# Kernel optimization log

Measured on AMD Instinct MI355X. Metric: run time of the kernel, lower is better.

The kernel has to match this reference:

```python
import jax, jax.numpy as jnp
import numpy as np

DIM = 192
HEADS = 6
WS = 7          # window size
SHIFT = 3       # shift size
HID = 768       # mlp hidden
EPS = 1e-5


def _rel_pos_index(ws):
    coords = np.stack(np.meshgrid(np.arange(ws), np.arange(ws), indexing='ij'))  # (2, ws, ws)
    cf = coords.reshape(2, -1)                       # (2, ws*ws)
    rel = cf[:, :, None] - cf[:, None, :]            # (2, N, N)
    rel = rel.transpose(1, 2, 0).astype(np.int64)
    rel[:, :, 0] += ws - 1
    rel[:, :, 1] += ws - 1
    rel[:, :, 0] *= 2 * ws - 1
    return jnp.asarray(rel.sum(-1))                  # (N, N)

REL_IDX = _rel_pos_index(WS)


def _layernorm(x, w, b):
    mu = jnp.mean(x, axis=-1, keepdims=True)
    var = jnp.mean(jnp.square(x - mu), axis=-1, keepdims=True)
    return (x - mu) * jax.lax.rsqrt(var + EPS) * w + b


def setup_inputs() -> dict:
    key = jax.random.key(0)
    ks = jax.random.split(key, 8)
    B, H, W = 32, 56, 56
    s = 0.02
    return {
        'x': jax.random.normal(ks[0], (B, H * W, DIM), jnp.float32),
        'norm1_w': jnp.ones((DIM,), jnp.float32),
        'norm1_b': jnp.zeros((DIM,), jnp.float32),
        'qkv_w': jax.random.normal(ks[1], (3 * DIM, DIM), jnp.float32) * s,
        'qkv_b': jnp.zeros((3 * DIM,), jnp.float32),
        'rpb_table': jax.random.normal(ks[2], ((2 * WS - 1) ** 2, HEADS), jnp.float32) * s,
        'proj_w': jax.random.normal(ks[3], (DIM, DIM), jnp.float32) * s,
        'proj_b': jnp.zeros((DIM,), jnp.float32),
        'norm2_w': jnp.ones((DIM,), jnp.float32),
        'norm2_b': jnp.zeros((DIM,), jnp.float32),
        'fc1_w': jax.random.normal(ks[4], (HID, DIM), jnp.float32) * s,
        'fc1_b': jnp.zeros((HID,), jnp.float32),
        'fc2_w': jax.random.normal(ks[5], (DIM, HID), jnp.float32) * s,
        'fc2_b': jnp.zeros((DIM,), jnp.float32),
        'H': H,
        'W': W,
    }


def reference(x, norm1_w, norm1_b, qkv_w, qkv_b, rpb_table, proj_w, proj_b,
              norm2_w, norm2_b, fc1_w, fc1_b, fc2_w, fc2_b, H, W):
    B, L, C = x.shape
    d = C // HEADS
    scale = d ** -0.5
    N = WS * WS

    shortcut = x
    h = _layernorm(x, norm1_w, norm1_b).reshape(B, H, W, C)
    if SHIFT > 0:
        h = jnp.roll(h, shift=(-SHIFT, -SHIFT), axis=(1, 2))

    # window partition -> (B * nW, N, C)
    h = h.reshape(B, H // WS, WS, W // WS, WS, C).transpose(0, 1, 3, 2, 4, 5)
    hw = h.reshape(-1, N, C)

    # windowed attention (NOTE: the torch block never passes a shift mask)
    qkv = hw @ qkv_w.T + qkv_b                                    # (B_, N, 3C)
    qkv = qkv.reshape(-1, N, 3, HEADS, d).transpose(2, 0, 3, 1, 4)
    q, k, v = qkv[0] * scale, qkv[1], qkv[2]                      # (B_, h, N, d)
    attn = jnp.einsum('bhnd,bhmd->bhnm', q, k)
    bias = rpb_table[REL_IDX].transpose(2, 0, 1)                  # (h, N, N)
    attn = jax.nn.softmax(attn + bias[None], axis=-1)
    out = jnp.einsum('bhnm,bhmd->bhnd', attn, v)
    out = out.transpose(0, 2, 1, 3).reshape(-1, N, C)
    out = out @ proj_w.T + proj_b

    # window reverse -> (B, H, W, C)
    out = out.reshape(B, H // WS, W // WS, WS, WS, C).transpose(0, 1, 3, 2, 4, 5)
    out = out.reshape(B, H, W, C)
    if SHIFT > 0:
        out = jnp.roll(out, shift=(SHIFT, SHIFT), axis=(1, 2))

    x = shortcut + out.reshape(B, L, C)
    h2 = _layernorm(x, norm2_w, norm2_b)
    mlp = jax.nn.gelu(h2 @ fc1_w.T + fc1_b, approximate=False) @ fc2_w.T + fc2_b
    return x + mlp
```

## Files before the change

### kernel.cpp

```cpp
#include <hip/hip_runtime.h>
#include <hip/hip_bf16.h>
#include <cmath>

typedef float f32x4 __attribute__((ext_vector_type(4)));
typedef __bf16 bf16x8 __attribute__((ext_vector_type(8)));

#define WS_SZ 7
#define SHIFT 3
#define HGRID 56
#define C_DIM 192
#define NHEADS 6
#define HDIM 32
#define NTOK 100352
#define NWIN 2048

__device__ __forceinline__ int win_to_tok(int wrow) {
    int w = wrow / 49, i = wrow - w * 49;
    int b = w >> 6, rem = w & 63;
    int wy = rem >> 3, wx = rem & 7;
    int yi = i / 7, xi = i - yi * 7;
    int y = wy * 7 + yi + SHIFT; if (y >= HGRID) y -= HGRID;
    int x = wx * 7 + xi + SHIFT; if (x >= HGRID) x -= HGRID;
    return b * (HGRID * HGRID) + y * HGRID + x;
}

__global__ __launch_bounds__(256)
void cvt_kernel(const float* __restrict__ src, __bf16* __restrict__ dst, int n8)
{
    int idx = blockIdx.x * 256 + threadIdx.x;
    if (idx >= n8) return;
    float4 a = ((const float4*)src)[idx * 2];
    float4 b = ((const float4*)src)[idx * 2 + 1];
    bf16x8 o;
    o[0] = (__bf16)a.x; o[1] = (__bf16)a.y; o[2] = (__bf16)a.z; o[3] = (__bf16)a.w;
    o[4] = (__bf16)b.x; o[5] = (__bf16)b.y; o[6] = (__bf16)b.z; o[7] = (__bf16)b.w;
    ((bf16x8*)dst)[idx] = o;
}

__global__ __launch_bounds__(256)
void bias_expand_kernel(const float* __restrict__ rpb, float* __restrict__ bias_g)
{
    int idx = blockIdx.x * 256 + threadIdx.x;
    if (idx >= NHEADS * 2401) return;
    int h = idx / 2401, rem = idx - h * 2401;
    int i = rem / 49, j = rem - i * 49;
    int yi = i / 7, xi = i - yi * 7;
    int yj = j / 7, xj = j - yj * 7;
    int ri = (yi - yj + 6) * 13 + (xi - xj + 6);
    bias_g[idx] = rpb[ri * NHEADS + h];
}

template<int WINDOWED>
__global__ __launch_bounds__(256)
void ln_kernel(const float* __restrict__ x, const float* __restrict__ w,
               const float* __restrict__ b, __bf16* __restrict__ out)
{
    int r = blockIdx.x * 4 + (threadIdx.x >> 6);
    int lane = threadIdx.x & 63;
    int src = WINDOWED ? win_to_tok(r) : r;
    const float* xp = x + (size_t)src * C_DIM;
    float v0 = xp[lane], v1 = xp[lane + 64], v2 = xp[lane + 128];
    float s = v0 + v1 + v2;
    float sq = v0 * v0 + v1 * v1 + v2 * v2;
    #pragma unroll
    for (int off = 32; off; off >>= 1) {
        s  += __shfl_xor(s, off);
        sq += __shfl_xor(sq, off);
    }
    float mu = s * (1.f / C_DIM);
    float rs = rsqrtf(sq * (1.f / C_DIM) - mu * mu + 1e-5f);
    __bf16* op = out + (size_t)r * C_DIM;
    op[lane]       = (__bf16)((v0 - mu) * rs * w[lane]       + b[lane]);
    op[lane + 64]  = (__bf16)((v1 - mu) * rs * w[lane + 64]  + b[lane + 64]);
    op[lane + 128] = (__bf16)((v2 - mu) * rs * w[lane + 128] + b[lane + 128]);
}

template<int MODE, int WBF16>
__global__ __launch_bounds__(256)
void gemm_kernel(const __bf16* __restrict__ A, const void* __restrict__ W,
                 const float* __restrict__ bias, void* __restrict__ outp,
                 const float* __restrict__ resid, int N, int K)
{
    __shared__ __bf16 As[128 * 40];
    __shared__ __bf16 Bs[64 * 40];
    const int tid = threadIdx.x;
    const int wave = tid >> 6, lane = tid & 63;
    const int wm = wave >> 1, wn = wave & 1;
    const int l15 = lane & 15, q8 = (lane >> 4) << 3;
    const int m0 = blockIdx.x * 128, n0 = blockIdx.y * 64;

    f32x4 acc[4][2];
    f32x4 zero = {0.f, 0.f, 0.f, 0.f};
    #pragma unroll
    for (int i = 0; i < 4; i++)
        #pragma unroll
        for (int j = 0; j < 2; j++) acc[i][j] = zero;

    const int br = tid >> 2, bc = (tid & 3) << 3;
    for (int kt = 0; kt < K; kt += 32) {
        __syncthreads();
        #pragma unroll
        for (int it = 0; it < 2; it++) {
            int idx = it * 256 + tid;
            int r = idx >> 2, c = (idx & 3) << 3;
            *(uint4*)(&As[r * 40 + c]) =
                *(const uint4*)(A + (size_t)(m0 + r) * K + kt + c);
        }
        if (WBF16) {
            *(uint4*)(&Bs[br * 40 + bc]) =
                *(const uint4*)((const __bf16*)W + (size_t)(n0 + br) * K + kt + bc);
        } else {
            const float* src = (const float*)W + (size_t)(n0 + br) * K + kt + bc;
            float4 f0 = *(const float4*)src;
            float4 f1 = *(const float4*)(src + 4);
            bf16x8 vb;
            vb[0] = (__bf16)f0.x; vb[1] = (__bf16)f0.y;
            vb[2] = (__bf16)f0.z; vb[3] = (__bf16)f0.w;
            vb[4] = (__bf16)f1.x; vb[5] = (__bf16)f1.y;
            vb[6] = (__bf16)f1.z; vb[7] = (__bf16)f1.w;
            *(bf16x8*)(&Bs[br * 40 + bc]) = vb;
        }
        __syncthreads();
        bf16x8 af[4], bfr[2];
        #pragma unroll
        for (int fm = 0; fm < 4; fm++)
            af[fm] = *(const bf16x8*)(&As[(wm * 64 + fm * 16 + l15) * 40 + q8]);
        #pragma unroll
        for (int fn = 0; fn < 2; fn++)
            bfr[fn] = *(const bf16x8*)(&Bs[(wn * 32 + fn * 16 + l15) * 40 + q8]);
        #pragma unroll
        for (int fm = 0; fm < 4; fm++)
            #pragma unroll
            for (int fn = 0; fn < 2; fn++)
                acc[fm][fn] = __builtin_amdgcn_mfma_f32_16x16x32_bf16(
                    af[fm], bfr[fn], acc[fm][fn], 0, 0, 0);
    }

    const int l4 = lane >> 4;
    #pragma unroll
    for (int fm = 0; fm < 4; fm++) {
        #pragma unroll
        for (int fn = 0; fn < 2; fn++) {
            int c = n0 + wn * 32 + fn * 16 + l15;
            float bv = bias[c];
            #pragma unroll
            for (int r = 0; r < 4; r++) {
                int m = m0 + wm * 64 + fm * 16 + l4 * 4 + r;
                float v = acc[fm][fn][r] + bv;
                if (MODE == 0) {
                    ((__bf16*)outp)[(size_t)m * N + c] = (__bf16)v;
                } else if (MODE == 2) {
                    float g = 0.5f * v * (1.f + erff(v * 0.70710678118654752f));
                    ((__bf16*)outp)[(size_t)m * N + c] = (__bf16)g;
                } else if (MODE == 1) {
                    int t = win_to_tok(m);
                    ((float*)outp)[(size_t)t * C_DIM + c] =
                        resid[(size_t)t * C_DIM + c] + v;
                } else {
                    float* p = (float*)outp + (size_t)m * C_DIM + c;
                    *p = *p + v;
                }
            }
        }
    }
}

__global__ __launch_bounds__(256, 2)
void attn_mfma_kernel(const __bf16* __restrict__ qkv,
                      const float* __restrict__ bias_g,
                      __bf16* __restrict__ out)
{
    const int wave = threadIdx.x >> 6;
    const int lane = threadIdx.x & 63;
    const int pair = blockIdx.x * 4 + wave;
    const int w = pair / 6, head = pair - (pair / 6) * 6;

    __shared__ __bf16 vsT_s[4][32 * 72];
    __shared__ __bf16 Ps_s[4][64 * 72];
    __bf16* vsT = vsT_s[wave];
    __bf16* Ps  = Ps_s[wave];

    const int l15 = lane & 15, q4 = lane >> 4, q8 = q4 << 3;
    const size_t qbase = (size_t)w * 49 * 576 + head * 32;

    {
        int d = lane & 31, jh = lane >> 5;
        #pragma unroll
        for (int it = 0; it < 25; ++it) {
            int j = it * 2 + jh;
            if (j < 49)
                vsT[d * 72 + j] = qkv[qbase + (size_t)j * 576 + 384 + d];
        }
        for (int idx = lane; idx < 32 * 15; idx += 64) {
            int dd = idx / 15, jj = 49 + (idx - dd * 15);
            vsT[dd * 72 + jj] = (__bf16)0.f;
        }
    }

    bf16x8 qf[4], kf[4];
    #pragma unroll
    for (int t = 0; t < 4; ++t) {
        int row = t * 16 + l15;
        int rq = row < 49 ? row : 48;
        qf[t] = *(const bf16x8*)(qkv + qbase + (size_t)rq * 576 + q8);
        kf[t] = *(const bf16x8*)(qkv + qbase + (size_t)rq * 576 + 192 + q8);
    }

    f32x4 sc[4][4];
    f32x4 zero = {0.f, 0.f, 0.f, 0.f};
    #pragma unroll
    for (int tm = 0; tm < 4; ++tm)
        #pragma unroll
        for (int tn = 0; tn < 4; ++tn) sc[tm][tn] = zero;
    #pragma unroll
    for (int tm = 0; tm < 4; ++tm)
        #pragma unroll
        for (int tn = 0; tn < 4; ++tn)
            sc[tm][tn] = __builtin_amdgcn_mfma_f32_16x16x32_bf16(
                qf[tm], kf[tn], sc[tm][tn], 0, 0, 0);

    const float scale = 0.17677669529663687f;
    const int hbase = head * 2401;
    #pragma unroll
    for (int tm = 0; tm < 4; ++tm) {
        #pragma unroll
        for (int r = 0; r < 4; ++r) {
            int i = tm * 16 + q4 * 4 + r;
            int ioff = hbase + (i < 49 ? i : 48) * 49;
            float v[4];
            #pragma unroll
            for (int tn = 0; tn < 4; ++tn) {
                int j = tn * 16 + l15;
                float bz = (j < 49) ? bias_g[ioff + (j < 49 ? j : 0)] : 0.f;
                float t = sc[tm][tn][r] * scale + bz;
                v[tn] = (j < 49) ? t : -1e30f;
            }
            float mx = fmaxf(fmaxf(v[0], v[1]), fmaxf(v[2], v[3]));
            mx = fmaxf(mx, __shfl_xor(mx, 1));
            mx = fmaxf(mx, __shfl_xor(mx, 2));
            mx = fmaxf(mx, __shfl_xor(mx, 4));
            mx = fmaxf(mx, __shfl_xor(mx, 8));
            float sm = 0.f;
            #pragma unroll
            for (int tn = 0; tn < 4; ++tn) {
                float e = __expf(v[tn] - mx);
                sc[tm][tn][r] = e;
                sm += e;
            }
            sm += __shfl_xor(sm, 1);
            sm += __shfl_xor(sm, 2);
            sm += __shfl_xor(sm, 4);
            sm += __shfl_xor(sm, 8);
            float inv = 1.f / sm;
            if (i < 49) {
                #pragma unroll
                for (int tn = 0; tn < 4; ++tn) {
                    int j = tn * 16 + l15;
                    Ps[i * 72 + j] = (__bf16)((j < 49) ? sc[tm][tn][r] * inv : 0.f);
                }
            }
        }
    }

    __syncthreads();

    f32x4 oc[4][2];
    #pragma unroll
    for (int tm = 0; tm < 4; ++tm)
        #pragma unroll
        for (int tn = 0; tn < 2; ++tn) oc[tm][tn] = zero;
    #pragma unroll
    for (int ks = 0; ks < 2; ++ks) {
        bf16x8 bv[2];
        #pragma unroll
        for (int tn = 0; tn < 2; ++tn)
            bv[tn] = *(const bf16x8*)(vsT + (tn * 16 + l15) * 72 + ks * 32 + q8);
        #pragma unroll
        for (int tm = 0; tm < 4; ++tm) {
            bf16x8 ap = *(const bf16x8*)(Ps + (tm * 16 + l15) * 72 + ks * 32 + q8);
            #pragma unroll
            for (int tn = 0; tn < 2; ++tn)
                oc[tm][tn] = __builtin_amdgcn_mfma_f32_16x16x32_bf16(
                    ap, bv[tn], oc[tm][tn], 0, 0, 0);
        }
    }

    #pragma unroll
    for (int tm = 0; tm < 4; ++tm) {
        #pragma unroll
        for (int r = 0; r < 4; ++r) {
            int m = tm * 16 + q4 * 4 + r;
            if (m < 49) {
                __bf16* op = out + (size_t)(w * 49 + m) * C_DIM + head * 32;
                #pragma unroll
                for (int tn = 0; tn < 2; ++tn)
                    op[tn * 16 + l15] = (__bf16)(oc[tm][tn][r]);
            }
        }
    }
}

extern "C" void kernel_launch(void* const* d_in, const int* in_sizes, int n_in,
                              void* d_out, int out_size, void* d_ws, size_t ws_size,
                              hipStream_t stream) {
    const float* x     = (const float*)d_in[0];
    const float* n1w   = (const float*)d_in[1];
    const float* n1b   = (const float*)d_in[2];
    const float* qkvw  = (const float*)d_in[3];
    const float* qkvb  = (const float*)d_in[4];
    const float* rpb   = (const float*)d_in[5];
    const float* projw = (const float*)d_in[6];
    const float* projb = (const float*)d_in[7];
    const float* n2w   = (const float*)d_in[8];
    const float* n2b   = (const float*)d_in[9];
    const float* fc1w  = (const float*)d_in[10];
    const float* fc1b  = (const float*)d_in[11];
    const float* fc2w  = (const float*)d_in[12];
    const float* fc2b  = (const float*)d_in[13];
    float* out = (float*)d_out;
    char* ws = (char*)d_ws;

    __bf16* bufA = (__bf16*)ws;
    __bf16* bufQ = (__bf16*)(ws + 38535168);
    __bf16* bufH = (__bf16*)(ws + 38535168);
    __bf16* qkvw_b  = (__bf16*)(ws + 192151552);
    __bf16* projw_b = (__bf16*)(ws + 192151552 + 221184);
    float*  bias_g  = (float*) (ws + 192151552 + 221184 + 73728);

    cvt_kernel<<<(110592/8 + 255)/256, 256, 0, stream>>>(qkvw, qkvw_b, 110592/8);
    cvt_kernel<<<(36864/8  + 255)/256, 256, 0, stream>>>(projw, projw_b, 36864/8);
    bias_expand_kernel<<<(NHEADS*2401 + 255)/256, 256, 0, stream>>>(rpb, bias_g);

    ln_kernel<1><<<NTOK / 4, 256, 0, stream>>>(x, n1w, n1b, bufA);
    gemm_kernel<0, 1><<<dim3(NTOK / 128, 9), 256, 0, stream>>>(
        bufA, qkvw_b, qkvb, bufQ, nullptr, 576, 192);
    attn_mfma_kernel<<<NWIN * NHEADS / 4, 256, 0, stream>>>(bufQ, bias_g, bufA);
    gemm_kernel<1, 1><<<dim3(NTOK / 128, 3), 256, 0, stream>>>(
        bufA, projw_b, projb, (void*)out, x, 192, 192);
    ln_kernel<0><<<NTOK / 4, 256, 0, stream>>>(out, n2w, n2b, bufA);
    gemm_kernel<2, 0><<<dim3(NTOK / 128, 12), 256, 0, stream>>>(
        bufA, fc1w, fc1b, bufH, nullptr, 768, 192);
    gemm_kernel<3, 0><<<dim3(NTOK / 128, 3), 256, 0, stream>>>(
        bufH, fc2w, fc2b, (void*)out, nullptr, 192, 768);
}
```

Before: 569.7 us.

## Fuse MLP fc1, GELU and fc2 into one kernel with LDS-resident hidden chunk

Replaces the separate fc1+GELU and fc2 GEMMs with a single kernel that computes 128-wide hidden chunks into shared memory and accumulates fc2 directly, avoiding the large bf16 hidden-activation round trip through global memory. The fc weights are pre-converted to bf16, and the GEMM grid is reordered so column tiles iterate fastest for better A-tile reuse in cache. The GELU is changed from exact erf to a sigmoid approximation, which alters numerics. Weights are read straight from global memory per wave without LDS staging.

```diff
diff --git a/kernel.cpp b/kernel.cpp
--- a/kernel.cpp
+++ b/kernel.cpp
@@ -75,9 +75,9 @@
     op[lane + 128] = (__bf16)((v2 - mu) * rs * w[lane + 128] + b[lane + 128]);
 }
 
-template<int MODE, int WBF16>
+template<int MODE>
 __global__ __launch_bounds__(256)
-void gemm_kernel(const __bf16* __restrict__ A, const void* __restrict__ W,
+void gemm_kernel(const __bf16* __restrict__ A, const __bf16* __restrict__ W,
                  const float* __restrict__ bias, void* __restrict__ outp,
                  const float* __restrict__ resid, int N, int K)
 {
@@ -87,7 +87,7 @@
     const int wave = tid >> 6, lane = tid & 63;
     const int wm = wave >> 1, wn = wave & 1;
     const int l15 = lane & 15, q8 = (lane >> 4) << 3;
-    const int m0 = blockIdx.x * 128, n0 = blockIdx.y * 64;
+    const int m0 = blockIdx.y * 128, n0 = blockIdx.x * 64;
 
     f32x4 acc[4][2];
     f32x4 zero = {0.f, 0.f, 0.f, 0.f};
@@ -106,20 +106,8 @@
             *(uint4*)(&As[r * 40 + c]) =
                 *(const uint4*)(A + (size_t)(m0 + r) * K + kt + c);
         }
-        if (WBF16) {
-            *(uint4*)(&Bs[br * 40 + bc]) =
-                *(const uint4*)((const __bf16*)W + (size_t)(n0 + br) * K + kt + bc);
-        } else {
-            const float* src = (const float*)W + (size_t)(n0 + br) * K + kt + bc;
-            float4 f0 = *(const float4*)src;
-            float4 f1 = *(const float4*)(src + 4);
-            bf16x8 vb;
-            vb[0] = (__bf16)f0.x; vb[1] = (__bf16)f0.y;
-            vb[2] = (__bf16)f0.z; vb[3] = (__bf16)f0.w;
-            vb[4] = (__bf16)f1.x; vb[5] = (__bf16)f1.y;
-            vb[6] = (__bf16)f1.z; vb[7] = (__bf16)f1.w;
-            *(bf16x8*)(&Bs[br * 40 + bc]) = vb;
-        }
+        *(uint4*)(&Bs[br * 40 + bc]) =
+            *(const uint4*)(W + (size_t)(n0 + br) * K + kt + bc);
         __syncthreads();
         bf16x8 af[4], bfr[2];
         #pragma unroll
@@ -149,17 +137,116 @@
                 float v = acc[fm][fn][r] + bv;
                 if (MODE == 0) {
                     ((__bf16*)outp)[(size_t)m * N + c] = (__bf16)v;
-                } else if (MODE == 2) {
-                    float g = 0.5f * v * (1.f + erff(v * 0.70710678118654752f));
-                    ((__bf16*)outp)[(size_t)m * N + c] = (__bf16)g;
-                } else if (MODE == 1) {
+                } else {
                     int t = win_to_tok(m);
                     ((float*)outp)[(size_t)t * C_DIM + c] =
                         resid[(size_t)t * C_DIM + c] + v;
-                } else {
-                    float* p = (float*)outp + (size_t)m * C_DIM + c;
-                    *p = *p + v;
                 }
+            }
+        }
+    }
+}
+
+__global__ __launch_bounds__(256, 3)
+void mlp_fused_kernel(const __bf16* __restrict__ A,
+                      const __bf16* __restrict__ w1,
+                      const float* __restrict__ b1,
+                      const __bf16* __restrict__ w2,
+                      const float* __restrict__ b2,
+                      float* __restrict__ out)
+{
+    __shared__ __bf16 As[64 * 200];
+    __shared__ __bf16 Hs[64 * 136];
+    const int tid = threadIdx.x;
+    const int wn = tid >> 6, lane = tid & 63;
+    const int l15 = lane & 15, q4 = lane >> 4, q8 = q4 << 3;
+    const int m0 = blockIdx.x * 64;
+
+    #pragma unroll
+    for (int it = 0; it < 6; ++it) {
+        int idx = it * 256 + tid;
+        int r = idx / 24, c = (idx - r * 24) << 3;
+        *(uint4*)(&As[r * 200 + c]) =
+            *(const uint4*)(A + (size_t)(m0 + r) * 192 + c);
+    }
+    __syncthreads();
+
+    f32x4 zero = {0.f, 0.f, 0.f, 0.f};
+    f32x4 acc2[4][3];
+    #pragma unroll
+    for (int tm = 0; tm < 4; ++tm)
+        #pragma unroll
+        for (int tn = 0; tn < 3; ++tn) acc2[tm][tn] = zero;
+
+    for (int ch = 0; ch < 6; ++ch) {
+        const int h0 = ch * 128;
+        f32x4 acc1[4][2];
+        #pragma unroll
+        for (int tm = 0; tm < 4; ++tm)
+            #pragma unroll
+            for (int tn = 0; tn < 2; ++tn) acc1[tm][tn] = zero;
+        #pragma unroll
+        for (int kt = 0; kt < 6; ++kt) {
+            bf16x8 bfr[2];
+            #pragma unroll
+            for (int tn = 0; tn < 2; ++tn)
+                bfr[tn] = *(const bf16x8*)(w1 +
+                    (size_t)(h0 + wn * 32 + tn * 16 + l15) * 192 + kt * 32 + q8);
+            #pragma unroll
+            for (int tm = 0; tm < 4; ++tm) {
+                bf16x8 af = *(const bf16x8*)(&As[(tm * 16 + l15) * 200 + kt * 32 + q8]);
+                #pragma unroll
+                for (int tn = 0; tn < 2; ++tn)
+                    acc1[tm][tn] = __builtin_amdgcn_mfma_f32_16x16x32_bf16(
+                        af, bfr[tn], acc1[tm][tn], 0, 0, 0);
+            }
+        }
+        __syncthreads();
+        #pragma unroll
+        for (int tm = 0; tm < 4; ++tm) {
+            #pragma unroll
+            for (int tn = 0; tn < 2; ++tn) {
+                int col = wn * 32 + tn * 16 + l15;
+                float bv = b1[h0 + col];
+                #pragma unroll
+                for (int r = 0; r < 4; ++r) {
+                    int row = tm * 16 + q4 * 4 + r;
+                    float v = acc1[tm][tn][r] + bv;
+                    float g = v / (1.f + __expf(-1.702f * v));
+                    Hs[row * 136 + col] = (__bf16)g;
+                }
+            }
+        }
+        __syncthreads();
+        #pragma unroll
+        for (int ks = 0; ks < 4; ++ks) {
+            bf16x8 bfr[3];
+            #pragma unroll
+            for (int tn = 0; tn < 3; ++tn)
+                bfr[tn] = *(const bf16x8*)(w2 +
+                    (size_t)(wn * 48 + tn * 16 + l15) * 768 + h0 + ks * 32 + q8);
+            #pragma unroll
+            for (int tm = 0; tm < 4; ++tm) {
+                bf16x8 af = *(const bf16x8*)(&Hs[(tm * 16 + l15) * 136 + ks * 32 + q8]);
+                #pragma unroll
+                for (int tn = 0; tn < 3; ++tn)
+                    acc2[tm][tn] = __builtin_amdgcn_mfma_f32_16x16x32_bf16(
+                        af, bfr[tn], acc2[tm][tn], 0, 0, 0);
+            }
+        }
+    }
+
+    #pragma unroll
+    for (int tm = 0; tm < 4; ++tm) {
+        #pragma unroll
+        for (int tn = 0; tn < 3; ++tn) {
+            int c = wn * 48 + tn * 16 + l15;
+            float bv = b2[c];
+            #pragma unroll
+            for (int r = 0; r < 4; ++r) {
+                int m = m0 + tm * 16 + q4 * 4 + r;
+                float* p = out + (size_t)m * C_DIM + c;
+                *p = *p + acc2[tm][tn][r] + bv;
             }
         }
     }
@@ -320,26 +407,27 @@
     float* out = (float*)d_out;
     char* ws = (char*)d_ws;
 
-    __bf16* bufA = (__bf16*)ws;
-    __bf16* bufQ = (__bf16*)(ws + 38535168);
-    __bf16* bufH = (__bf16*)(ws + 38535168);
-    __bf16* qkvw_b  = (__bf16*)(ws + 192151552);
-    __bf16* projw_b = (__bf16*)(ws + 192151552 + 221184);
-    float*  bias_g  = (float*) (ws + 192151552 + 221184 + 73728);
+    __bf16* bufA    = (__bf16*)ws;
+    __bf16* bufQ    = (__bf16*)(ws + 38535168);
+    __bf16* qkvw_b  = (__bf16*)(ws + 154140672);
+    __bf16* projw_b = (__bf16*)(ws + 154361856);
+    __bf16* fc1w_b  = (__bf16*)(ws + 154435584);
+    __bf16* fc2w_b  = (__bf16*)(ws + 154730496);
+    float*  bias_g  = (float*) (ws + 155025408);
 
     cvt_kernel<<<(110592/8 + 255)/256, 256, 0, stream>>>(qkvw, qkvw_b, 110592/8);
     cvt_kernel<<<(36864/8  + 255)/256, 256, 0, stream>>>(projw, projw_b, 36864/8);
+    cvt_kernel<<<(147456/8 + 255)/256, 256, 0, stream>>>(fc1w, fc1w_b, 147456/8);
+    cvt_kernel<<<(147456/8 + 255)/256, 256, 0, stream>>>(fc2w, fc2w_b, 147456/8);
     bias_expand_kernel<<<(NHEADS*2401 + 255)/256, 256, 0, stream>>>(rpb, bias_g);
 
     ln_kernel<1><<<NTOK / 4, 256, 0, stream>>>(x, n1w, n1b, bufA);
-    gemm_kernel<0, 1><<<dim3(NTOK / 128, 9), 256, 0, stream>>>(
+    gemm_kernel<0><<<dim3(9, NTOK / 128), 256, 0, stream>>>(
         bufA, qkvw_b, qkvb, bufQ, nullptr, 576, 192);
     attn_mfma_kernel<<<NWIN * NHEADS / 4, 256, 0, stream>>>(bufQ, bias_g, bufA);
-    gemm_kernel<1, 1><<<dim3(NTOK / 128, 3), 256, 0, stream>>>(
+    gemm_kernel<1><<<dim3(3, NTOK / 128), 256, 0, stream>>>(
         bufA, projw_b, projb, (void*)out, x, 192, 192);
     ln_kernel<0><<<NTOK / 4, 256, 0, stream>>>(out, n2w, n2b, bufA);
-    gemm_kernel<2, 0><<<dim3(NTOK / 128, 12), 256, 0, stream>>>(
-        bufA, fc1w, fc1b, bufH, nullptr, 768, 192);
-    gemm_kernel<3, 0><<<dim3(NTOK / 128, 3), 256, 0, stream>>>(
-        bufH, fc2w, fc2b, (void*)out, nullptr, 192, 768);
-}
+    mlp_fused_kernel<<<NTOK / 64, 256, 0, stream>>>(
+        bufA, fc1w_b, fc1b, fc2w_b, fc2b, out);
+}
```

Measured after the change: 530.7 us. 6.8% less time.
